# Kernel optimization log

Hardware: AMD Instinct MI355X
Metric: run time of the kernel (lower is better)

The kernel has to match this reference:

```python
import jax, jax.numpy as jnp
import numpy as np

N_NODES = 50000
N_EDGES = 800000
IN_CH, HID_CH, OUT_CH = 512, 128, 64


def gcn_conv(x, W, b, src, dst, num_nodes):
    """PyG GCNConv: add self-loops, sym-normalize, linear, scatter-add, bias.
    x: [N, Fin], W: [Fout, Fin], b: [Fout], src/dst: [E] int."""
    loop = jnp.arange(num_nodes, dtype=src.dtype)
    src2 = jnp.concatenate([src, loop])  # [E+N]
    dst2 = jnp.concatenate([dst, loop])
    deg = jax.ops.segment_sum(jnp.ones_like(dst2, dtype=x.dtype), dst2,
                              num_segments=num_nodes)  # in-degree + 1
    d_inv_sqrt = jnp.where(deg > 0, jax.lax.rsqrt(deg), 0.0)
    norm = d_inv_sqrt[src2] * d_inv_sqrt[dst2]  # [E+N]
    h = x @ W.T  # [N, Fout]
    msg = h[src2] * norm[:, None]  # [E+N, Fout] -- dominant memory traffic
    out = jax.ops.segment_sum(msg, dst2, num_segments=num_nodes)
    return out + b


def setup_inputs() -> dict:
    key = jax.random.key(0)
    ks = jax.random.split(key, 8)
    x = jax.random.normal(ks[0], (N_NODES, IN_CH), dtype=jnp.float32)
    edge_index = jax.random.randint(ks[1], (2, N_EDGES), 0, N_NODES, dtype=jnp.int64)
    s1 = 1.0 / np.sqrt(IN_CH)
    s2 = 1.0 / np.sqrt(HID_CH)
    W1 = jax.random.normal(ks[2], (HID_CH, IN_CH), dtype=jnp.float32) * s1
    b1 = jnp.zeros((HID_CH,), dtype=jnp.float32)
    W_mu = jax.random.normal(ks[3], (OUT_CH, HID_CH), dtype=jnp.float32) * s2
    b_mu = jnp.zeros((OUT_CH,), dtype=jnp.float32)
    W_logstd = jax.random.normal(ks[4], (OUT_CH, HID_CH), dtype=jnp.float32) * s2
    b_logstd = jnp.zeros((OUT_CH,), dtype=jnp.float32)
    return {"x": x, "edge_index": edge_index, "W1": W1, "b1": b1,
            "W_mu": W_mu, "b_mu": b_mu, "W_logstd": W_logstd, "b_logstd": b_logstd}


def reference(x, edge_index, W1, b1, W_mu, b_mu, W_logstd, b_logstd):
    src, dst = edge_index[0], edge_index[1]
    n = x.shape[0]
    h = jax.nn.relu(gcn_conv(x, W1, b1, src, dst, n))
    mu = gcn_conv(h, W_mu, b_mu, src, dst, n)
    logstd = gcn_conv(h, W_logstd, b_logstd, src, dst, n)
    return (mu, logstd)
```

## Files before the change

kernel.cpp:

```cpp
#include <hip/hip_runtime.h>

constexpr int FIN = 512;
constexpr int FH  = 128;
constexpr int FO  = 64;

typedef short short8 __attribute__((ext_vector_type(8)));
typedef float f32x4 __attribute__((ext_vector_type(4)));

__device__ __forceinline__ unsigned short f2bf(float f) {
    unsigned u = __float_as_uint(f);
    u += 0x7fffu + ((u >> 16) & 1u);
    return (unsigned short)(u >> 16);
}
__device__ __forceinline__ float bf2f(unsigned short h) {
    return __uint_as_float((unsigned)h << 16);
}


__global__ void convw1_kernel(const float* __restrict__ W, unsigned short* __restrict__ Wb,
                              int n4) {
    int i = blockIdx.x * blockDim.x + threadIdx.x;
    if (i < n4) {
        float4 v = ((const float4*)W)[i];
        ushort4 p;
        p.x = f2bf(v.x); p.y = f2bf(v.y); p.z = f2bf(v.z); p.w = f2bf(v.w);
        ((ushort4*)Wb)[i] = p;
    }
}

__global__ void convw2_kernel(const float* __restrict__ Wmu, const float* __restrict__ Wlg,
                              unsigned short* __restrict__ Wh, unsigned short* __restrict__ Wl) {
    int i = blockIdx.x * blockDim.x + threadIdx.x;
    if (i < 128 * 128) {
        int r = i >> 7, c = i & 127;
        float f = (r < 64) ? Wmu[r * 128 + c] : Wlg[(r - 64) * 128 + c];
        unsigned short h = f2bf(f);
        Wh[i] = h;
        Wl[i] = f2bf(f - bf2f(h));
    }
}


__global__ void count_kernel(const int* __restrict__ dst, int* __restrict__ cnt, int E) {
    int i = blockIdx.x * blockDim.x + threadIdx.x;
    if (i < E) atomicAdd(&cnt[dst[i]], 1);
}

__global__ void dinv_kernel(const int* __restrict__ cnt, float* __restrict__ dinv, int n) {
    int i = blockIdx.x * blockDim.x + threadIdx.x;
    if (i < n) dinv[i] = rsqrtf((float)(cnt[i] + 1));
}


__global__ void scan1_kernel(const int* __restrict__ cnt, int* __restrict__ offs,
                             int* __restrict__ bsum, int n) {
    __shared__ int sdata[256];
    int t = threadIdx.x;
    int base = blockIdx.x * 1024 + t * 4;
    int4 c = make_int4(0, 0, 0, 0);
    if (base + 3 < n) {
        c = *(const int4*)(cnt + base);
    } else {
        if (base + 0 < n) c.x = cnt[base + 0];
        if (base + 1 < n) c.y = cnt[base + 1];
        if (base + 2 < n) c.z = cnt[base + 2];
        if (base + 3 < n) c.w = cnt[base + 3];
    }
    int s0 = c.x + c.y + c.z + c.w;
    sdata[t] = s0;
    __syncthreads();
    for (int off = 1; off < 256; off <<= 1) {
        int v = (t >= off) ? sdata[t - off] : 0;
        __syncthreads();
        sdata[t] += v;
        __syncthreads();
    }
    int excl = sdata[t] - s0;
    if (t == 255) bsum[blockIdx.x] = sdata[255];
    if (base + 0 < n) offs[base + 0] = excl;
    if (base + 1 < n) offs[base + 1] = excl + c.x;
    if (base + 2 < n) offs[base + 2] = excl + c.x + c.y;
    if (base + 3 < n) offs[base + 3] = excl + c.x + c.y + c.z;
}

__global__ void scan2_kernel(int* __restrict__ bsum, int nb) {
    __shared__ int sdata[256];
    int t = threadIdx.x;
    int v = (t < nb) ? bsum[t] : 0;
    sdata[t] = v;
    __syncthreads();
    for (int off = 1; off < 256; off <<= 1) {
        int u = (t >= off) ? sdata[t - off] : 0;
        __syncthreads();
        sdata[t] += u;
        __syncthreads();
    }
    if (t < nb) bsum[t] = sdata[t] - v;
}

__global__ void scan3_kernel(int* __restrict__ offs, const int* __restrict__ bsum,
                             int n, int E) {
    int i = blockIdx.x * blockDim.x + threadIdx.x;
    if (i < n) offs[i] += bsum[i >> 10];
    if (i == 0) offs[n] = E;
}


__global__ void fill_kernel(const int* __restrict__ src, const int* __restrict__ dst,
                            const float* __restrict__ dinv, const int* __restrict__ offs,
                            int* __restrict__ cursor, int2* __restrict__ esort, int E) {
    int i = blockIdx.x * blockDim.x + threadIdx.x;
    if (i < E) {
        int s = src[i];
        int d = dst[i];
        int pos = offs[d] + atomicAdd(&cursor[d], 1);
        float w = dinv[s] * dinv[d];
        esort[pos] = make_int2(s, __float_as_int(w));
    }
}


__global__ void spmm_kernel(const unsigned int* __restrict__ hin, const int* __restrict__ offs,
                            const int2* __restrict__ esort, const float* __restrict__ dinv,
                            const float* __restrict__ bias, void* __restrict__ hout,
                            int n, int obf) {
    int gid = blockIdx.x * blockDim.x + threadIdx.x;
    int node = gid >> 6;
    int lane = threadIdx.x & 63;
    if (node >= n) return;
    float di = dinv[node];
    unsigned hv = hin[(size_t)node * 64 + lane];
    float ax = di * di * __uint_as_float(hv << 16);
    float ay = di * di * __uint_as_float(hv & 0xffff0000u);
    int p = offs[node];
    int end = offs[node + 1];
    for (; p + 4 <= end; p += 4) {
        int2 e0 = esort[p + 0];
        int2 e1 = esort[p + 1];
        int2 e2 = esort[p + 2];
        int2 e3 = esort[p + 3];
        unsigned v0 = hin[(size_t)e0.x * 64 + lane];
        unsigned v1 = hin[(size_t)e1.x * 64 + lane];
        unsigned v2 = hin[(size_t)e2.x * 64 + lane];
        unsigned v3 = hin[(size_t)e3.x * 64 + lane];
        float w0 = __int_as_float(e0.y), w1 = __int_as_float(e1.y);
        float w2 = __int_as_float(e2.y), w3 = __int_as_float(e3.y);
        ax = fmaf(w0, __uint_as_float(v0 << 16), ax);
        ay = fmaf(w0, __uint_as_float(v0 & 0xffff0000u), ay);
        ax = fmaf(w1, __uint_as_float(v1 << 16), ax);
        ay = fmaf(w1, __uint_as_float(v1 & 0xffff0000u), ay);
        ax = fmaf(w2, __uint_as_float(v2 << 16), ax);
        ay = fmaf(w2, __uint_as_float(v2 & 0xffff0000u), ay);
        ax = fmaf(w3, __uint_as_float(v3 << 16), ax);
        ay = fmaf(w3, __uint_as_float(v3 & 0xffff0000u), ay);
    }
    for (; p < end; ++p) {
        int2 e = esort[p];
        unsigned v = hin[(size_t)e.x * 64 + lane];
        float w = __int_as_float(e.y);
        ax = fmaf(w, __uint_as_float(v << 16), ax);
        ay = fmaf(w, __uint_as_float(v & 0xffff0000u), ay);
    }
    if (bias) {
        float2 b = ((const float2*)bias)[lane];
        ax += b.x; ay += b.y;
    }
    if (obf) {
        ax = fmaxf(ax, 0.f); ay = fmaxf(ay, 0.f);
        unsigned o = (unsigned)f2bf(ax) | ((unsigned)f2bf(ay) << 16);
        ((unsigned*)hout)[(size_t)node * 64 + lane] = o;
    } else {
        float2 o; o.x = ax; o.y = ay;
        ((float2*)hout)[(size_t)node * 64 + lane] = o;
    }
}


__global__ __launch_bounds__(256, 3) void gemm1_kernel(
    const float* __restrict__ X, const unsigned short* __restrict__ Wb,
    unsigned short* __restrict__ out, int M) {
    __shared__ __align__(16) unsigned short As[2][64 * 64];
    __shared__ __align__(16) unsigned short Bs[2][128 * 64];

    int tid = threadIdx.x;
    int lane = tid & 63, wid = tid >> 6;
    int fr = lane & 15, fq = lane >> 4;
    int row0 = blockIdx.x * 64;

    int a_r = tid >> 4, a_kq = tid & 15;
    int b_r = tid >> 3, b_c = tid & 7;

    f32x4 acc[8] = {};
    float4 a_reg[4];
    short8 b_reg[4];

    auto issue = [&](int k0) {
        #pragma unroll
        for (int j = 0; j < 4; ++j) {
            int ar = a_r + 16 * j;
            int grow = row0 + ar; if (grow >= M) grow = M - 1;
            a_reg[j] = *(const float4*)(X + (size_t)grow * FIN + k0 + a_kq * 4);
            int br = b_r + 32 * j;
            b_reg[j] = *(const short8*)(Wb + (size_t)br * FIN + k0 + b_c * 8);
        }
    };
    auto commit = [&](int buf) {
        #pragma unroll
        for (int j = 0; j < 4; ++j) {
            int ar = a_r + 16 * j;
            ushort4 p;
            p.x = f2bf(a_reg[j].x); p.y = f2bf(a_reg[j].y);
            p.z = f2bf(a_reg[j].z); p.w = f2bf(a_reg[j].w);
            *(ushort4*)((char*)As[buf] + ar * 128 + ((a_kq * 8) ^ ((ar & 7) << 4))) = p;
            int br = b_r + 32 * j;
            *(short8*)((char*)Bs[buf] + br * 128 + ((b_c * 16) ^ ((br & 7) << 4))) = b_reg[j];
        }
    };
    auto compute = [&](int buf) {
        #pragma unroll
        for (int s = 0; s < 2; ++s) {
            int r = wid * 16 + fr;
            short8 af = *(const short8*)((const char*)As[buf] + r * 128 +
                                         ((s * 64 + fq * 16) ^ ((r & 7) << 4)));
            #pragma unroll
            for (int c = 0; c < 8; ++c) {
                int br = c * 16 + fr;
                short8 bfr = *(const short8*)((const char*)Bs[buf] + br * 128 +
                                              ((s * 64 + fq * 16) ^ ((br & 7) << 4)));
                acc[c] = __builtin_amdgcn_mfma_f32_16x16x32_bf16(af, bfr, acc[c], 0, 0, 0);
            }
        }
    };

    issue(0);
    commit(0);
    __syncthreads();
    for (int kk = 0; kk < 7; ++kk) {
        issue((kk + 1) * 64);
        compute(kk & 1);
        __syncthreads();
        commit((kk + 1) & 1);
        __syncthreads();
    }
    compute(1);

    #pragma unroll
    for (int c = 0; c < 8; ++c) {
        #pragma unroll
        for (int j = 0; j < 4; ++j) {
            int row = row0 + wid * 16 + fq * 4 + j;
            if (row < M) out[(size_t)row * FH + c * 16 + fr] = f2bf(acc[c][j]);
        }
    }
}


__global__ __launch_bounds__(512) void gemm2_kernel(
    const float* __restrict__ X,
    const unsigned short* __restrict__ Wh, const unsigned short* __restrict__ Wl,
    float* __restrict__ outA, float* __restrict__ outB,
    const float* __restrict__ biasA, const float* __restrict__ biasB,
    int M, int nstrips) {
    __shared__ __align__(16) unsigned short WhS[128 * 128];
    __shared__ __align__(16) unsigned short WlS[128 * 128];
    int tid = threadIdx.x;

    #pragma unroll
    for (int j = 0; j < 4; ++j) {
        int f = tid + j * 512;
        int row = f >> 4;
        unsigned addr = ((unsigned)f * 16u) ^ ((unsigned)(row & 7) << 4);
        *(short8*)((char*)WhS + addr) = ((const short8*)Wh)[f];
        *(short8*)((char*)WlS + addr) = ((const short8*)Wl)[f];
    }
    __syncthreads();

    int lane = tid & 63, wid = tid >> 6;
    int fr = lane & 15, fq = lane >> 4;
    int s = blockIdx.x * 8 + wid;
    if (s >= nstrips) return;
    int row0 = s * 16;
    int arow = row0 + fr; if (arow > M - 1) arow = M - 1;
    const float* ap = X + (size_t)arow * FH + fq * 8;

    float4 a0 = *(const float4*)(ap + 0);
    float4 a1 = *(const float4*)(ap + 4);
    float4 a2 = *(const float4*)(ap + 32);
    float4 a3 = *(const float4*)(ap + 36);
    float4 a4 = *(const float4*)(ap + 64);
    float4 a5 = *(const float4*)(ap + 68);
    float4 a6 = *(const float4*)(ap + 96);
    float4 a7 = *(const float4*)(ap + 100);

    f32x4 acc[8] = {};

    auto proc = [&](int k0, float4 c0, float4 c1) {
        float a[8] = {c0.x, c0.y, c0.z, c0.w, c1.x, c1.y, c1.z, c1.w};
        short8 ah, al;
        #pragma unroll
        for (int i = 0; i < 8; ++i) {
            unsigned short h = f2bf(a[i]);
            ah[i] = (short)h;
            al[i] = (short)f2bf(a[i] - bf2f(h));
        }
        int cb = k0 * 2 + fq * 16;
        #pragma unroll
        for (int c = 0; c < 8; ++c) {
            int lr = c * 16 + fr;
            unsigned addr = ((unsigned)(lr * 256 + cb)) ^ ((unsigned)(lr & 7) << 4);
            short8 bh = *(const short8*)((const char*)WhS + addr);
            short8 bl = *(const short8*)((const char*)WlS + addr);
            acc[c] = __builtin_amdgcn_mfma_f32_16x16x32_bf16(ah, bh, acc[c], 0, 0, 0);
            acc[c] = __builtin_amdgcn_mfma_f32_16x16x32_bf16(al, bh, acc[c], 0, 0, 0);
            acc[c] = __builtin_amdgcn_mfma_f32_16x16x32_bf16(ah, bl, acc[c], 0, 0, 0);
        }
    };
    proc(0, a0, a1);
    proc(32, a2, a3);
    proc(64, a4, a5);
    proc(96, a6, a7);

    #pragma unroll
    for (int c = 0; c < 8; ++c) {
        float* outp = (c < 4) ? outA : outB;
        const float* bp = (c < 4) ? biasA : biasB;
        int col = (c & 3) * 16 + fr;
        float bv = bp[col];
        #pragma unroll
        for (int j = 0; j < 4; ++j) {
            int row = row0 + fq * 4 + j;
            if (row < M) outp[(size_t)row * FO + col] = acc[c][j] + bv;
        }
    }
}


extern "C" void kernel_launch(void* const* d_in, const int* in_sizes, int n_in,
                              void* d_out, int out_size, void* d_ws, size_t ws_size,
                              hipStream_t stream) {
    const float* x   = (const float*)d_in[0];
    const int*   ei  = (const int*)d_in[1];
    const float* W1  = (const float*)d_in[2];
    const float* b1  = (const float*)d_in[3];
    const float* Wmu = (const float*)d_in[4];
    const float* bmu = (const float*)d_in[5];
    const float* Wlg = (const float*)d_in[6];
    const float* blg = (const float*)d_in[7];

    const int n = in_sizes[0] / FIN;
    const int E = in_sizes[1] / 2;
    const int* src = ei;
    const int* dst = ei + E;
    const int nstrips = (n + 15) / 16;

    char* ws = (char*)d_ws;
    size_t off = 0;
    auto alloc = [&](size_t bytes) -> void* {
        void* p = ws + off;
        off = (off + bytes + 255) & ~((size_t)255);
        return p;
    };
    int*   cnt    = (int*)  alloc((size_t)n * 4);
    int*   offs   = (int*)  alloc((size_t)(n + 1) * 4);
    int*   cursor = (int*)  alloc((size_t)n * 4);
    int*   bsum   = (int*)  alloc(1024);
    float* dinv   = (float*)alloc((size_t)n * 4);
    int2*  esort  = (int2*) alloc((size_t)E * 8);
    unsigned short* hbf  = (unsigned short*)alloc((size_t)n * FH * 2);
    unsigned short* h1bf = (unsigned short*)alloc((size_t)n * FH * 2);
    float* ah2    = (float*)alloc((size_t)n * FH * 4);
    unsigned short* W1b = (unsigned short*)alloc((size_t)FH * FIN * 2);
    unsigned short* W2h = (unsigned short*)alloc((size_t)FH * FH * 2);
    unsigned short* W2l = (unsigned short*)alloc((size_t)FH * FH * 2);

    hipMemsetAsync(cnt, 0, (size_t)n * 4, stream);
    hipMemsetAsync(cursor, 0, (size_t)n * 4, stream);

    convw1_kernel<<<(FH * FIN / 4 + 255) / 256, 256, 0, stream>>>(W1, W1b, FH * FIN / 4);
    convw2_kernel<<<(FH * FH + 255) / 256, 256, 0, stream>>>(Wmu, Wlg, W2h, W2l);

    count_kernel<<<(E + 255) / 256, 256, 0, stream>>>(dst, cnt, E);
    dinv_kernel<<<(n + 255) / 256, 256, 0, stream>>>(cnt, dinv, n);

    int nb = (n + 1023) / 1024;
    scan1_kernel<<<nb, 256, 0, stream>>>(cnt, offs, bsum, n);
    scan2_kernel<<<1, 256, 0, stream>>>(bsum, nb);
    scan3_kernel<<<(n + 255) / 256, 256, 0, stream>>>(offs, bsum, n, E);

    fill_kernel<<<(E + 255) / 256, 256, 0, stream>>>(src, dst, dinv, offs, cursor, esort, E);

    gemm1_kernel<<<(n + 63) / 64, 256, 0, stream>>>(x, W1b, hbf, n);
    spmm_kernel<<<(n + 3) / 4, 256, 0, stream>>>(
        (const unsigned*)hbf, offs, esort, dinv, b1, h1bf, n, 1);
    spmm_kernel<<<(n + 3) / 4, 256, 0, stream>>>(
        (const unsigned*)h1bf, offs, esort, dinv, nullptr, ah2, n, 0);
    float* outmu = (float*)d_out;
    float* outlg = outmu + (size_t)n * FO;
    gemm2_kernel<<<512, 512, 0, stream>>>(ah2, W2h, W2l, outmu, outlg, bmu, blg, n, nstrips);
}
```

Before: 217.7 us.

## Store second aggregation in bf16 and rework gemm1 double-buffer pipeline

The second SpMM now writes its aggregated features as bf16 instead of fp32. gemm2 reads these directly, which drops the hi/lo split of the activation and one of its three MFMAs per tile. This halves the intermediate write and read traffic and trims gemm2 compute, at the cost of rounding the aggregated activations to bf16. Separately, gemm1's loop issues global loads two stages ahead and uses a single barrier per iteration instead of two, to overlap loads with compute better.

```diff
diff --git a/kernel.cpp b/kernel.cpp
--- a/kernel.cpp
+++ b/kernel.cpp
@@ -122,8 +122,8 @@
 
 __global__ void spmm_kernel(const unsigned int* __restrict__ hin, const int* __restrict__ offs,
                             const int2* __restrict__ esort, const float* __restrict__ dinv,
-                            const float* __restrict__ bias, void* __restrict__ hout,
-                            int n, int obf) {
+                            const float* __restrict__ bias, unsigned int* __restrict__ hout,
+                            int n, int relu) {
     int gid = blockIdx.x * blockDim.x + threadIdx.x;
     int node = gid >> 6;
     int lane = threadIdx.x & 63;
@@ -165,14 +165,9 @@
         float2 b = ((const float2*)bias)[lane];
         ax += b.x; ay += b.y;
     }
-    if (obf) {
-        ax = fmaxf(ax, 0.f); ay = fmaxf(ay, 0.f);
-        unsigned o = (unsigned)f2bf(ax) | ((unsigned)f2bf(ay) << 16);
-        ((unsigned*)hout)[(size_t)node * 64 + lane] = o;
-    } else {
-        float2 o; o.x = ax; o.y = ay;
-        ((float2*)hout)[(size_t)node * 64 + lane] = o;
-    }
+    if (relu) { ax = fmaxf(ax, 0.f); ay = fmaxf(ay, 0.f); }
+    unsigned o = (unsigned)f2bf(ax) | ((unsigned)f2bf(ay) << 16);
+    hout[(size_t)node * 64 + lane] = o;
 }
 
 
@@ -234,15 +229,14 @@
 
     issue(0);
     commit(0);
+    issue(64);
     __syncthreads();
-    for (int kk = 0; kk < 7; ++kk) {
-        issue((kk + 1) * 64);
+    for (int kk = 0; kk < 8; ++kk) {
         compute(kk & 1);
-        __syncthreads();
-        commit((kk + 1) & 1);
-        __syncthreads();
-    }
-    compute(1);
+        if (kk < 7) commit((kk + 1) & 1);
+        if (kk < 6) issue((kk + 2) * 64);
+        __syncthreads();
+    }
 
     #pragma unroll
     for (int c = 0; c < 8; ++c) {
@@ -256,7 +250,7 @@
 
 
 __global__ __launch_bounds__(512) void gemm2_kernel(
-    const float* __restrict__ X,
+    const unsigned short* __restrict__ Xb,
     const unsigned short* __restrict__ Wh, const unsigned short* __restrict__ Wl,
     float* __restrict__ outA, float* __restrict__ outB,
     const float* __restrict__ biasA, const float* __restrict__ biasB,
@@ -281,28 +275,16 @@
     if (s >= nstrips) return;
     int row0 = s * 16;
     int arow = row0 + fr; if (arow > M - 1) arow = M - 1;
-    const float* ap = X + (size_t)arow * FH + fq * 8;
-
-    float4 a0 = *(const float4*)(ap + 0);
-    float4 a1 = *(const float4*)(ap + 4);
-    float4 a2 = *(const float4*)(ap + 32);
-    float4 a3 = *(const float4*)(ap + 36);
-    float4 a4 = *(const float4*)(ap + 64);
-    float4 a5 = *(const float4*)(ap + 68);
-    float4 a6 = *(const float4*)(ap + 96);
-    float4 a7 = *(const float4*)(ap + 100);
+    const unsigned short* ap = Xb + (size_t)arow * FH + fq * 8;
+
+    short8 a0 = *(const short8*)(ap + 0);
+    short8 a1 = *(const short8*)(ap + 32);
+    short8 a2 = *(const short8*)(ap + 64);
+    short8 a3 = *(const short8*)(ap + 96);
 
     f32x4 acc[8] = {};
 
-    auto proc = [&](int k0, float4 c0, float4 c1) {
-        float a[8] = {c0.x, c0.y, c0.z, c0.w, c1.x, c1.y, c1.z, c1.w};
-        short8 ah, al;
-        #pragma unroll
-        for (int i = 0; i < 8; ++i) {
-            unsigned short h = f2bf(a[i]);
-            ah[i] = (short)h;
-            al[i] = (short)f2bf(a[i] - bf2f(h));
-        }
+    auto proc = [&](int k0, short8 a) {
         int cb = k0 * 2 + fq * 16;
         #pragma unroll
         for (int c = 0; c < 8; ++c) {
@@ -310,15 +292,14 @@
             unsigned addr = ((unsigned)(lr * 256 + cb)) ^ ((unsigned)(lr & 7) << 4);
             short8 bh = *(const short8*)((const char*)WhS + addr);
             short8 bl = *(const short8*)((const char*)WlS + addr);
-            acc[c] = __builtin_amdgcn_mfma_f32_16x16x32_bf16(ah, bh, acc[c], 0, 0, 0);
-            acc[c] = __builtin_amdgcn_mfma_f32_16x16x32_bf16(al, bh, acc[c], 0, 0, 0);
-            acc[c] = __builtin_amdgcn_mfma_f32_16x16x32_bf16(ah, bl, acc[c], 0, 0, 0);
-        }
-    };
-    proc(0, a0, a1);
-    proc(32, a2, a3);
-    proc(64, a4, a5);
-    proc(96, a6, a7);
+            acc[c] = __builtin_amdgcn_mfma_f32_16x16x32_bf16(a, bh, acc[c], 0, 0, 0);
+            acc[c] = __builtin_amdgcn_mfma_f32_16x16x32_bf16(a, bl, acc[c], 0, 0, 0);
+        }
+    };
+    proc(0, a0);
+    proc(32, a1);
+    proc(64, a2);
+    proc(96, a3);
 
     #pragma unroll
     for (int c = 0; c < 8; ++c) {
@@ -368,7 +349,7 @@
     int2*  esort  = (int2*) alloc((size_t)E * 8);
     unsigned short* hbf  = (unsigned short*)alloc((size_t)n * FH * 2);
     unsigned short* h1bf = (unsigned short*)alloc((size_t)n * FH * 2);
-    float* ah2    = (float*)alloc((size_t)n * FH * 4);
+    unsigned short* ah2b = (unsigned short*)alloc((size_t)n * FH * 2);
     unsigned short* W1b = (unsigned short*)alloc((size_t)FH * FIN * 2);
     unsigned short* W2h = (unsigned short*)alloc((size_t)FH * FH * 2);
     unsigned short* W2l = (unsigned short*)alloc((size_t)FH * FH * 2);
@@ -391,10 +372,10 @@
 
     gemm1_kernel<<<(n + 63) / 64, 256, 0, stream>>>(x, W1b, hbf, n);
     spmm_kernel<<<(n + 3) / 4, 256, 0, stream>>>(
-        (const unsigned*)hbf, offs, esort, dinv, b1, h1bf, n, 1);
+        (const unsigned*)hbf, offs, esort, dinv, b1, (unsigned*)h1bf, n, 1);
     spmm_kernel<<<(n + 3) / 4, 256, 0, stream>>>(
-        (const unsigned*)h1bf, offs, esort, dinv, nullptr, ah2, n, 0);
+        (const unsigned*)h1bf, offs, esort, dinv, nullptr, (unsigned*)ah2b, n, 0);
     float* outmu = (float*)d_out;
     float* outlg = outmu + (size_t)n * FO;
-    gemm2_kernel<<<512, 512, 0, stream>>>(ah2, W2h, W2l, outmu, outlg, bmu, blg, n, nstrips);
-}
+    gemm2_kernel<<<512, 512, 0, stream>>>(ah2b, W2h, W2l, outmu, outlg, bmu, blg, n, nstrips);
+}
```

Measured after the change: 210.7 us. -3.2%, faster.
